# Kernel optimization log

Measured on AMD Instinct MI355X. Metric: run time of the kernel, lower is better.

The kernel has to match this reference:

```python
import jax, jax.numpy as jnp
import numpy as np

N = 50000          # nodes
E = 1_600_000      # edges (avg degree 32)
D_IN = 128
D_OUT = 128
K = 16             # SSGC hops
ALPHA = 0.05


def setup_inputs() -> dict:
    key = jax.random.key(0)
    k1, k2, k3 = jax.random.split(key, 3)
    node_emb = jax.random.normal(k1, (N, D_IN), dtype=jnp.float32)
    edge_index = jax.random.randint(k2, (2, E), 0, N, dtype=jnp.int32)
    # Parameters of SSGConv's internal Linear(in_channels, out_channels)
    weight = jax.random.normal(k3, (D_OUT, D_IN), dtype=jnp.float32) * (1.0 / np.sqrt(D_IN))
    bias = jnp.zeros((D_OUT,), dtype=jnp.float32)
    return {"node_emb": node_emb, "edge_index": edge_index, "weight": weight, "bias": bias}


def reference(node_emb, edge_index, weight, bias):
    n = node_emb.shape[0]
    # GCN normalization with self-loops (PyG gcn_norm, add_self_loops=True)
    loops = jnp.arange(n, dtype=edge_index.dtype)
    src = jnp.concatenate([edge_index[0], loops])  # [E+N]
    dst = jnp.concatenate([edge_index[1], loops])  # [E+N]
    ones = jnp.ones(src.shape[0], dtype=node_emb.dtype)
    deg = jax.ops.segment_sum(ones, dst, num_segments=n)           # in-degree incl. self-loop
    dinv = jnp.where(deg > 0, jax.lax.rsqrt(deg), 0.0)
    norm = dinv[src] * dinv[dst]                                   # [E+N]

    def prop(x):
        msgs = norm[:, None] * x[src]                              # [E+N, D]
        return jax.ops.segment_sum(msgs, dst, num_segments=n)

    # SSGConv: h = alpha*x0 + (1-alpha)/K * sum_{k=1..K} A_hat^k x0, then Linear
    def step(carry, _):
        x, h = carry
        x = prop(x)
        h = h + ((1.0 - ALPHA) / K) * x
        return (x, h), None

    (_, h), _ = jax.lax.scan(step, (node_emb, ALPHA * node_emb), None, length=K)
    out = h @ weight.T + bias
    # Dropout(p=0.5) is identity in eval mode
    return out
```

## Files before the change

kernel.cpp:

```cpp
#include <hip/hip_runtime.h>


#define N_NODES 50000
#define N_EDGES 1600000
#define D 128
#define K_HOPS 16
#define ALPHA 0.05f
#define HCOEF ((1.0f - ALPHA) / (float)K_HOPS)

__device__ __forceinline__ unsigned int f2bf(float f) {
    unsigned int u = __float_as_uint(f);
    return (u + 0x7FFFu + ((u >> 16) & 1u)) >> 16;
}
__device__ __forceinline__ unsigned int pack_bf2(float x, float y) {
    return f2bf(x) | (f2bf(y) << 16);
}
__device__ __forceinline__ float bf_lo(unsigned int w) { return __uint_as_float(w << 16); }
__device__ __forceinline__ float bf_hi(unsigned int w) { return __uint_as_float(w & 0xFFFF0000u); }

__global__ void deg_kernel(const int* __restrict__ dst, int* __restrict__ deg,
                           int* __restrict__ rank, int e) {
    int i = blockIdx.x * blockDim.x + threadIdx.x;
    if (i < e) rank[i] = atomicAdd(&deg[dst[i]], 1);
}

__global__ void dinv_kernel(const int* __restrict__ deg, float* __restrict__ dinv,
                            float* __restrict__ selfw, int n) {
    int i = blockIdx.x * blockDim.x + threadIdx.x;
    if (i < n) {
        float di = rsqrtf((float)(deg[i] + 1));
        dinv[i] = di;
        selfw[i] = di * di;
    }
}

__global__ void scan_kernel(const int* __restrict__ deg, int* __restrict__ row_start, int n) {
    __shared__ int wsum[16];
    __shared__ int tot_s;
    __shared__ int carry_s;
    int tid = threadIdx.x, lane = tid & 63, wid = tid >> 6;
    if (tid == 0) carry_s = 0;
    __syncthreads();
    for (int base = 0; base < n; base += 1024) {
        int i = base + tid;
        int v = (i < n) ? deg[i] : 0;
        int s = v;
        #pragma unroll
        for (int off = 1; off < 64; off <<= 1) {
            int t = __shfl_up(s, off, 64);
            if (lane >= off) s += t;
        }
        if (lane == 63) wsum[wid] = s;
        __syncthreads();
        if (tid == 0) {
            int run = 0;
            #pragma unroll
            for (int w = 0; w < 16; ++w) { int t = wsum[w]; wsum[w] = run; run += t; }
            tot_s = run;
        }
        __syncthreads();
        if (i < n) row_start[i] = carry_s + wsum[wid] + (s - v);
        __syncthreads();
        if (tid == 0) carry_s += tot_s;
    }
    __syncthreads();
    if (tid == 0) row_start[n] = carry_s;
}

__global__ void scatter_kernel(const int* __restrict__ src, const int* __restrict__ dst,
                               const int* __restrict__ rank,
                               const int* __restrict__ row_start, int2* __restrict__ csr,
                               const float* __restrict__ dinv, int e) {
    int i = blockIdx.x * blockDim.x + threadIdx.x;
    if (i < e) {
        int d = dst[i];
        int s = src[i];
        int pos = row_start[d] + rank[i];
        csr[pos] = make_int2(s, __float_as_int(dinv[d] * dinv[s]));
    }
}

__global__ void init_kernel(const float2* __restrict__ x0, unsigned int* __restrict__ xb,
                            float2* __restrict__ h, int n2) {
    int i = blockIdx.x * blockDim.x + threadIdx.x;
    if (i < n2) {
        float2 v = x0[i];
        xb[i] = pack_bf2(v.x, v.y);
        h[i] = make_float2(ALPHA * v.x, ALPHA * v.y);
    }
}

#define GATHER_BLOCK(W)                                                         \
    {                                                                           \
        unsigned int g[W];                                                      \
        float wv[W];                                                            \
        _Pragma("unroll") for (int q = 0; q < W; ++q) {                         \
            int s = __shfl(rec.x, j + q);                                       \
            wv[q] = __int_as_float(__shfl(rec.y, j + q));                       \
            g[q] = xb[(size_t)s * 64 + lane];                                   \
        }                                                                       \
        _Pragma("unroll") for (int q = 0; q < W; ++q) {                         \
            accx += wv[q] * bf_lo(g[q]);                                        \
            accy += wv[q] * bf_hi(g[q]);                                        \
        }                                                                       \
        j += W;                                                                 \
    }

__global__ __launch_bounds__(256) void agg_kernel(
    const unsigned int* __restrict__ xb, unsigned int* __restrict__ yb,
    float2* __restrict__ h2, const float* __restrict__ selfw,
    const int* __restrict__ row_start, const int2* __restrict__ csr, int update_h) {
    int wid = threadIdx.x >> 6;
    int lane = threadIdx.x & 63;
    int node = blockIdx.x * 4 + wid;
    if (node >= N_NODES) return;

    int r0 = row_start[node];
    int r1 = row_start[node + 1];
    int deg = r1 - r0;
    size_t o = (size_t)node * 64 + lane;

    unsigned int vw = xb[o];
    float sw = selfw[node];
    float accx = sw * bf_lo(vw), accy = sw * bf_hi(vw);

    for (int base = 0; base < deg; base += 64) {
        int cnt = deg - base;
        if (cnt > 64) cnt = 64;
        int idx = r0 + base + lane;
        if (idx >= r1) idx = r1 - 1;
        int2 rec = csr[idx];

        int j = 0;
        while (j + 16 <= cnt) GATHER_BLOCK(16);
        if (j + 8 <= cnt) GATHER_BLOCK(8);
        if (j + 4 <= cnt) GATHER_BLOCK(4);
        for (; j < cnt; ++j) {
            int s = __shfl(rec.x, j);
            float w = __int_as_float(__shfl(rec.y, j));
            unsigned int gw = xb[(size_t)s * 64 + lane];
            accx += w * bf_lo(gw);
            accy += w * bf_hi(gw);
        }
    }

    yb[o] = pack_bf2(accx, accy);
    if (update_h) {
        float2 hv = h2[o];
        hv.x += HCOEF * (bf_lo(vw) + accx);
        hv.y += HCOEF * (bf_hi(vw) + accy);
        h2[o] = hv;
    }
}

__global__ __launch_bounds__(256) void gemm_kernel(
    const float* __restrict__ h, const float* __restrict__ w,
    const float* __restrict__ bias, float* __restrict__ out) {
    __shared__ float sAT[128][64];
    __shared__ float sBT[128][64];
    int tid = threadIdx.x;
    int row0 = blockIdx.x * 64;
    int col0 = blockIdx.y * 64;

    for (int idx = tid; idx < 64 * 32; idx += 256) {
        int r = idx & 63, kq = idx >> 6;
        float4 v;
        if (row0 + r < N_NODES)
            v = *(const float4*)&h[(size_t)(row0 + r) * D + kq * 4];
        else
            v = make_float4(0.f, 0.f, 0.f, 0.f);
        sAT[kq * 4 + 0][r] = v.x;
        sAT[kq * 4 + 1][r] = v.y;
        sAT[kq * 4 + 2][r] = v.z;
        sAT[kq * 4 + 3][r] = v.w;
    }
    for (int idx = tid; idx < 64 * 32; idx += 256) {
        int c = idx & 63, kq = idx >> 6;
        float4 v = *(const float4*)&w[(size_t)(col0 + c) * D + kq * 4];
        sBT[kq * 4 + 0][c] = v.x;
        sBT[kq * 4 + 1][c] = v.y;
        sBT[kq * 4 + 2][c] = v.z;
        sBT[kq * 4 + 3][c] = v.w;
    }
    __syncthreads();

    int cg = tid & 15;
    int rg = tid >> 4;
    float acc[4][4] = {};
    #pragma unroll 2
    for (int k = 0; k < 128; ++k) {
        float4 a = *(const float4*)&sAT[k][rg * 4];
        float4 b = *(const float4*)&sBT[k][cg * 4];
        acc[0][0] += a.x * b.x; acc[0][1] += a.x * b.y; acc[0][2] += a.x * b.z; acc[0][3] += a.x * b.w;
        acc[1][0] += a.y * b.x; acc[1][1] += a.y * b.y; acc[1][2] += a.y * b.z; acc[1][3] += a.y * b.w;
        acc[2][0] += a.z * b.x; acc[2][1] += a.z * b.y; acc[2][2] += a.z * b.z; acc[2][3] += a.z * b.w;
        acc[3][0] += a.w * b.x; acc[3][1] += a.w * b.y; acc[3][2] += a.w * b.z; acc[3][3] += a.w * b.w;
    }

    float4 bv = *(const float4*)&bias[col0 + cg * 4];
    #pragma unroll
    for (int i = 0; i < 4; ++i) {
        int r = row0 + rg * 4 + i;
        if (r < N_NODES) {
            float4 ov = make_float4(acc[i][0] + bv.x, acc[i][1] + bv.y,
                                    acc[i][2] + bv.z, acc[i][3] + bv.w);
            *(float4*)&out[(size_t)r * D + col0 + cg * 4] = ov;
        }
    }
}

extern "C" void kernel_launch(void* const* d_in, const int* in_sizes, int n_in,
                              void* d_out, int out_size, void* d_ws, size_t ws_size,
                              hipStream_t stream) {
    const float* node_emb = (const float*)d_in[0];
    const int*   edge     = (const int*)d_in[1];
    const float* weight   = (const float*)d_in[2];
    const float* bias     = (const float*)d_in[3];
    float* out = (float*)d_out;

    char* ws = (char*)d_ws;
    float*        hbuf = (float*)ws;        ws += (size_t)N_NODES * D * sizeof(float);
    unsigned int* xb0  = (unsigned int*)ws; ws += (size_t)N_NODES * 64 * sizeof(unsigned int);
    unsigned int* xb1  = (unsigned int*)ws; ws += (size_t)N_NODES * 64 * sizeof(unsigned int);
    int2*  csr      = (int2*)ws;  ws += (size_t)N_EDGES * sizeof(int2);
    int*   rank     = (int*)ws;   ws += (size_t)N_EDGES * sizeof(int);
    int*   deg      = (int*)ws;   ws += (size_t)N_NODES * sizeof(int);
    int*   row_start= (int*)ws;   ws += (size_t)(N_NODES + 1) * sizeof(int);
    float* dinv     = (float*)ws; ws += (size_t)N_NODES * sizeof(float);
    float* selfw    = (float*)ws; ws += (size_t)N_NODES * sizeof(float);

    const int* srcp = edge;
    const int* dstp = edge + N_EDGES;

    hipMemsetAsync(deg, 0, N_NODES * sizeof(int), stream);

    deg_kernel<<<(N_EDGES + 255) / 256, 256, 0, stream>>>(dstp, deg, rank, N_EDGES);
    dinv_kernel<<<(N_NODES + 255) / 256, 256, 0, stream>>>(deg, dinv, selfw, N_NODES);
    scan_kernel<<<1, 1024, 0, stream>>>(deg, row_start, N_NODES);
    scatter_kernel<<<(N_EDGES + 255) / 256, 256, 0, stream>>>(srcp, dstp, rank, row_start,
                                                              csr, dinv, N_EDGES);

    int n2 = N_NODES * D / 2;
    init_kernel<<<(n2 + 255) / 256, 256, 0, stream>>>((const float2*)node_emb, xb0,
                                                      (float2*)hbuf, n2);

    unsigned int* cur = xb0;
    unsigned int* nxt = xb1;
    for (int k = 0; k < K_HOPS; ++k) {
        agg_kernel<<<(N_NODES + 3) / 4, 256, 0, stream>>>(cur, nxt, (float2*)hbuf,
                                                          selfw, row_start, csr, k & 1);
        unsigned int* tmp = cur; cur = nxt; nxt = tmp;
    }

    dim3 ggrid((N_NODES + 63) / 64, 2);
    gemm_kernel<<<ggrid, 256, 0, stream>>>(hbuf, weight, bias, out);
}
```

Measured before the change: 1.104 ms.

## Fuse all propagation hops into one persistent cooperative kernel with grid sync

Replaces the per-hop launches and the init kernel with a single cooperative kernel of 625 blocks. Each wave owns 20 nodes and keeps their previous-hop values and h accumulators in registers, with a grid-wide barrier between hops. This removes 16 kernel launches and the per-hop global reads and writes of h and of the node's own row. In exchange occupancy is capped at one fixed grid of 2500 waves, the register arrays raise register pressure, and the grid syncs add barrier cost. If the cooperative launch fails it falls back to the old path.

```diff
diff --git a/kernel.cpp b/kernel.cpp
--- a/kernel.cpp
+++ b/kernel.cpp
@@ -1,4 +1,7 @@
 #include <hip/hip_runtime.h>
+#include <hip/hip_cooperative_groups.h>
+
+namespace cg = cooperative_groups;
 
 
 #define N_NODES 50000
@@ -7,6 +10,9 @@
 #define K_HOPS 16
 #define ALPHA 0.05f
 #define HCOEF ((1.0f - ALPHA) / (float)K_HOPS)
+
+#define NBLOCKS 625
+#define NODES_PER_WAVE 20
 
 __device__ __forceinline__ unsigned int f2bf(float f) {
     unsigned int u = __float_as_uint(f);
@@ -90,14 +96,14 @@
     }
 }
 
-#define GATHER_BLOCK(W)                                                         \
+#define GATHER_BLOCK(SRCBUF, W)                                                 \
     {                                                                           \
         unsigned int g[W];                                                      \
         float wv[W];                                                            \
         _Pragma("unroll") for (int q = 0; q < W; ++q) {                         \
             int s = __shfl(rec.x, j + q);                                       \
             wv[q] = __int_as_float(__shfl(rec.y, j + q));                       \
-            g[q] = xb[(size_t)s * 64 + lane];                                   \
+            g[q] = SRCBUF[(size_t)s * 64 + lane];                               \
         }                                                                       \
         _Pragma("unroll") for (int q = 0; q < W; ++q) {                         \
             accx += wv[q] * bf_lo(g[q]);                                        \
@@ -132,9 +138,9 @@
         int2 rec = csr[idx];
 
         int j = 0;
-        while (j + 16 <= cnt) GATHER_BLOCK(16);
-        if (j + 8 <= cnt) GATHER_BLOCK(8);
-        if (j + 4 <= cnt) GATHER_BLOCK(4);
+        while (j + 16 <= cnt) GATHER_BLOCK(xb, 16);
+        if (j + 8 <= cnt) GATHER_BLOCK(xb, 8);
+        if (j + 4 <= cnt) GATHER_BLOCK(xb, 4);
         for (; j < cnt; ++j) {
             int s = __shfl(rec.x, j);
             float w = __int_as_float(__shfl(rec.y, j));
@@ -150,6 +156,79 @@
         hv.x += HCOEF * (bf_lo(vw) + accx);
         hv.y += HCOEF * (bf_hi(vw) + accy);
         h2[o] = hv;
+    }
+}
+
+__global__ __launch_bounds__(256, 3) void hops_kernel(
+    const float2* __restrict__ x0, unsigned int* __restrict__ xa,
+    unsigned int* __restrict__ xb, float2* __restrict__ hout,
+    const float* __restrict__ selfw, const int* __restrict__ row_start,
+    const int2* __restrict__ csr) {
+    cg::grid_group grid = cg::this_grid();
+    int gwave = (int)((blockIdx.x * 256 + threadIdx.x) >> 6);
+    int lane = threadIdx.x & 63;
+    int node0 = gwave * NODES_PER_WAVE;
+
+    float hx[NODES_PER_WAVE], hy[NODES_PER_WAVE];
+    float px[NODES_PER_WAVE], py[NODES_PER_WAVE];
+
+    #pragma unroll
+    for (int n = 0; n < NODES_PER_WAVE; ++n) {
+        int node = node0 + n;
+        float2 v = x0[(size_t)node * 64 + lane];
+        px[n] = v.x; py[n] = v.y;
+        hx[n] = ALPHA * v.x; hy[n] = ALPHA * v.y;
+        xa[(size_t)node * 64 + lane] = pack_bf2(v.x, v.y);
+    }
+    __threadfence();
+    grid.sync();
+
+    unsigned int* cur = xa;
+    unsigned int* nxt = xb;
+    for (int k = 0; k < K_HOPS; ++k) {
+        #pragma unroll
+        for (int n = 0; n < NODES_PER_WAVE; ++n) {
+            int node = node0 + n;
+            int r0 = row_start[node];
+            int r1 = row_start[node + 1];
+            int deg = r1 - r0;
+            float sw = selfw[node];
+            float accx = sw * px[n], accy = sw * py[n];
+
+            for (int base = 0; base < deg; base += 64) {
+                int cnt = deg - base;
+                if (cnt > 64) cnt = 64;
+                int idx = r0 + base + lane;
+                if (idx >= r1) idx = r1 - 1;
+                int2 rec = csr[idx];
+
+                int j = 0;
+                while (j + 16 <= cnt) GATHER_BLOCK(cur, 16);
+                if (j + 8 <= cnt) GATHER_BLOCK(cur, 8);
+                if (j + 4 <= cnt) GATHER_BLOCK(cur, 4);
+                for (; j < cnt; ++j) {
+                    int s = __shfl(rec.x, j);
+                    float w = __int_as_float(__shfl(rec.y, j));
+                    unsigned int gw = cur[(size_t)s * 64 + lane];
+                    accx += w * bf_lo(gw);
+                    accy += w * bf_hi(gw);
+                }
+            }
+
+            hx[n] += HCOEF * accx;
+            hy[n] += HCOEF * accy;
+            px[n] = accx; py[n] = accy;
+            nxt[(size_t)node * 64 + lane] = pack_bf2(accx, accy);
+        }
+        __threadfence();
+        grid.sync();
+        unsigned int* t = cur; cur = nxt; nxt = t;
+    }
+
+    #pragma unroll
+    for (int n = 0; n < NODES_PER_WAVE; ++n) {
+        int node = node0 + n;
+        hout[(size_t)node * 64 + lane] = make_float2(hx[n], hy[n]);
     }
 }
 
@@ -184,27 +263,27 @@
     }
     __syncthreads();
 
-    int cg = tid & 15;
+    int cg2 = tid & 15;
     int rg = tid >> 4;
     float acc[4][4] = {};
     #pragma unroll 2
     for (int k = 0; k < 128; ++k) {
         float4 a = *(const float4*)&sAT[k][rg * 4];
-        float4 b = *(const float4*)&sBT[k][cg * 4];
+        float4 b = *(const float4*)&sBT[k][cg2 * 4];
         acc[0][0] += a.x * b.x; acc[0][1] += a.x * b.y; acc[0][2] += a.x * b.z; acc[0][3] += a.x * b.w;
         acc[1][0] += a.y * b.x; acc[1][1] += a.y * b.y; acc[1][2] += a.y * b.z; acc[1][3] += a.y * b.w;
         acc[2][0] += a.z * b.x; acc[2][1] += a.z * b.y; acc[2][2] += a.z * b.z; acc[2][3] += a.z * b.w;
         acc[3][0] += a.w * b.x; acc[3][1] += a.w * b.y; acc[3][2] += a.w * b.z; acc[3][3] += a.w * b.w;
     }
 
-    float4 bv = *(const float4*)&bias[col0 + cg * 4];
+    float4 bv = *(const float4*)&bias[col0 + cg2 * 4];
     #pragma unroll
     for (int i = 0; i < 4; ++i) {
         int r = row0 + rg * 4 + i;
         if (r < N_NODES) {
             float4 ov = make_float4(acc[i][0] + bv.x, acc[i][1] + bv.y,
                                     acc[i][2] + bv.z, acc[i][3] + bv.w);
-            *(float4*)&out[(size_t)r * D + col0 + cg * 4] = ov;
+            *(float4*)&out[(size_t)r * D + col0 + cg2 * 4] = ov;
         }
     }
 }
@@ -240,16 +319,23 @@
     scatter_kernel<<<(N_EDGES + 255) / 256, 256, 0, stream>>>(srcp, dstp, rank, row_start,
                                                               csr, dinv, N_EDGES);
 
-    int n2 = N_NODES * D / 2;
-    init_kernel<<<(n2 + 255) / 256, 256, 0, stream>>>((const float2*)node_emb, xb0,
-                                                      (float2*)hbuf, n2);
-
-    unsigned int* cur = xb0;
-    unsigned int* nxt = xb1;
-    for (int k = 0; k < K_HOPS; ++k) {
-        agg_kernel<<<(N_NODES + 3) / 4, 256, 0, stream>>>(cur, nxt, (float2*)hbuf,
-                                                          selfw, row_start, csr, k & 1);
-        unsigned int* tmp = cur; cur = nxt; nxt = tmp;
+    const float2* x0c = (const float2*)node_emb;
+    float2* houtc = (float2*)hbuf;
+    void* args[] = {(void*)&x0c, (void*)&xb0, (void*)&xb1, (void*)&houtc,
+                    (void*)&selfw, (void*)&row_start, (void*)&csr};
+    hipError_t cerr = hipLaunchCooperativeKernel((void*)hops_kernel, dim3(NBLOCKS), dim3(256),
+                                                 args, 0, stream);
+    if (cerr != hipSuccess) {
+        int n2 = N_NODES * D / 2;
+        init_kernel<<<(n2 + 255) / 256, 256, 0, stream>>>((const float2*)node_emb, xb0,
+                                                          (float2*)hbuf, n2);
+        unsigned int* cur = xb0;
+        unsigned int* nxt = xb1;
+        for (int k = 0; k < K_HOPS; ++k) {
+            agg_kernel<<<(N_NODES + 3) / 4, 256, 0, stream>>>(cur, nxt, (float2*)hbuf,
+                                                              selfw, row_start, csr, k & 1);
+            unsigned int* tmp = cur; cur = nxt; nxt = tmp;
+        }
     }
 
     dim3 ggrid((N_NODES + 63) / 64, 2);
```

Result: slower. 3.918 ms (+255.0%).
